# Kernel optimization log

Measured on AMD Instinct MI355X. Metric: run time of the kernel, lower is better.

The kernel has to match this reference:

```python
import jax, jax.numpy as jnp
import numpy as np

IN_FEATURES = 2048
HIDDEN_FEATURES = 8192  # = num_experts * expert_hidden
TOKENS = 16384


def setup_inputs() -> dict:
    key = jax.random.key(0)
    k1, k2, k3, k4 = jax.random.split(key, 4)
    scale = 1.0 / np.sqrt(IN_FEATURES)
    x = jax.random.normal(k1, (TOKENS, IN_FEATURES), dtype=jnp.float32)
    w1 = jax.random.normal(k2, (HIDDEN_FEATURES, IN_FEATURES), dtype=jnp.float32) * scale
    w2 = jax.random.normal(k3, (HIDDEN_FEATURES, IN_FEATURES), dtype=jnp.float32) * scale
    w3 = jax.random.normal(k4, (HIDDEN_FEATURES, IN_FEATURES), dtype=jnp.float32) * scale
    return {"x": x, "w1": w1, "w2": w2, "w3": w3, "num_experts": 8}


def reference(x, w1, w2, w3, num_experts):
    # Block-sparse MoE SwiGLU FFN. Tokens are sorted by expert and balanced:
    # token block e uses hidden slice e of w1/w2/w3 (the stk topology).
    tokens, d = x.shape
    hidden = w1.shape[0]
    e = num_experts
    h_e = hidden // e            # per-expert hidden size
    t_e = tokens // e            # tokens per expert
    xe = x.reshape(e, t_e, d)                  # [E, Te, D]
    w1e = w1.reshape(e, h_e, d)                # [E, He, D]
    w2e = w2.reshape(e, h_e, d)
    w3e = w3.reshape(e, h_e, d)
    # sdd: sparse output of x @ w^T restricted to each token's expert block
    h1 = jnp.einsum("etd,ehd->eth", xe, w1e)   # [E, Te, He]
    h2 = jnp.einsum("etd,ehd->eth", xe, w2e)
    g = jax.nn.silu(h1) * h2                   # fused SiLU gating
    # dsd: block-sparse @ dense w3 -> dense [tokens, D]
    out = jnp.einsum("eth,ehd->etd", g, w3e)
    return out.reshape(tokens, d)
```

## Files before the change

kernel.cpp:

```cpp
#include <hip/hip_runtime.h>
#include <stdint.h>


#define NEXP   8
#define TOKENS 16384
#define D_IN   2048
#define HIDDEN 8192
#define T_E    2048
#define H_E    1024

typedef __attribute__((ext_vector_type(8))) __bf16 bf16x8;
typedef __attribute__((ext_vector_type(4))) float  f32x4;

__device__ __forceinline__ void async_ld16(const void* g, void* l) {
  __builtin_amdgcn_global_load_lds(
      (const __attribute__((address_space(1))) void*)g,
      (__attribute__((address_space(3))) void*)l, 16, 0, 0);
}

__device__ __forceinline__ unsigned short f2bf(float f) {
  union { float f; uint32_t u; } c; c.f = f;
  uint32_t u = c.u;
  u += 0x7FFFu + ((u >> 16) & 1u);
  return (unsigned short)(u >> 16);
}

__device__ __forceinline__ void tile_swizzle(int s, int& mt, int& nt) {
  int g  = s >> 4;
  int w  = s & 15;
  int gm = g & 3, gn = g >> 2;
  int wm = w & 3, wn = w >> 2;
  mt = gm * 4 + wm;
  nt = gn * 4 + wn;
}

__global__ __launch_bounds__(256) void cvt_kernel(
    const float* __restrict__ in, unsigned short* __restrict__ out, int n4) {
  int i = blockIdx.x * 256 + threadIdx.x;
  if (i >= n4) return;
  float4 v = ((const float4*)in)[i];
  ushort4 r;
  r.x = f2bf(v.x); r.y = f2bf(v.y); r.z = f2bf(v.z); r.w = f2bf(v.w);
  ((ushort4*)out)[i] = r;
}

__global__ __launch_bounds__(256) void transpose_w3_kernel(
    const float* __restrict__ w3, unsigned short* __restrict__ w3t) {
  __shared__ unsigned short tile[32][33];
  const int d0 = blockIdx.x * 32;
  const int h0 = blockIdx.y * 32;
  const int tx = threadIdx.x;
  const int ty = threadIdx.y;
#pragma unroll
  for (int j = 0; j < 32; j += 8)
    tile[ty + j][tx] = f2bf(w3[(size_t)(h0 + ty + j) * D_IN + d0 + tx]);
  __syncthreads();
  const int e   = h0 >> 10;
  const int hl0 = h0 & 1023;
#pragma unroll
  for (int j = 0; j < 32; j += 8)
    w3t[((size_t)e * D_IN + d0 + ty + j) * H_E + hl0 + tx] = tile[tx][ty + j];
}

__global__ __launch_bounds__(256) void gemm1_kernel(
    const unsigned short* __restrict__ xb,
    const unsigned short* __restrict__ w1b,
    const unsigned short* __restrict__ w2b,
    unsigned short* __restrict__ g)
{
  __shared__ unsigned short As[128 * 32];
  __shared__ unsigned short B1s[64 * 32];
  __shared__ unsigned short B2s[64 * 32];

  const int bid = blockIdx.x;
  const int e   = bid & 7;
  const int s   = bid >> 3;
  int mt, nt;
  tile_swizzle(s, mt, nt);
  const int m0 = mt * 128;
  const int n0 = nt * 64;

  const unsigned short* A  = xb  + (size_t)e * T_E * D_IN;
  const unsigned short* B1 = w1b + (size_t)e * H_E * D_IN;
  const unsigned short* B2 = w2b + (size_t)e * H_E * D_IN;

  const int tid  = threadIdx.x;
  const int wave = tid >> 6;
  const int lane = tid & 63;
  const int wm   = wave >> 1;
  const int wn   = wave & 1;
  const int srow = lane >> 2;
  const int scol = (lane & 3) * 8;
  const int lm   = lane & 15;
  const int q8   = (lane >> 4) * 8;

  f32x4 acc1[4][2], acc2[4][2];
#pragma unroll
  for (int mi = 0; mi < 4; ++mi)
#pragma unroll
    for (int ni = 0; ni < 2; ++ni) {
      acc1[mi][ni] = (f32x4){0.f, 0.f, 0.f, 0.f};
      acc2[mi][ni] = (f32x4){0.f, 0.f, 0.f, 0.f};
    }

  for (int k0 = 0; k0 < D_IN; k0 += 32) {
    __syncthreads();
#pragma unroll
    for (int j = 0; j < 2; ++j) {
      int r = (wave * 2 + j) * 16 + srow;
      async_ld16(A + (size_t)(m0 + r) * D_IN + k0 + scol,
                 (char*)As + (wave * 2 + j) * 1024 + lane * 16);
    }
    {
      int r = wave * 16 + srow;
      async_ld16(B1 + (size_t)(n0 + r) * D_IN + k0 + scol,
                 (char*)B1s + wave * 1024 + lane * 16);
      async_ld16(B2 + (size_t)(n0 + r) * D_IN + k0 + scol,
                 (char*)B2s + wave * 1024 + lane * 16);
    }
    __syncthreads();

    bf16x8 af[4], b1f[2], b2f[2];
#pragma unroll
    for (int mi = 0; mi < 4; ++mi)
      af[mi] = *(const bf16x8*)(As + (wm * 64 + mi * 16 + lm) * 32 + q8);
#pragma unroll
    for (int ni = 0; ni < 2; ++ni) {
      b1f[ni] = *(const bf16x8*)(B1s + (wn * 32 + ni * 16 + lm) * 32 + q8);
      b2f[ni] = *(const bf16x8*)(B2s + (wn * 32 + ni * 16 + lm) * 32 + q8);
    }
#pragma unroll
    for (int mi = 0; mi < 4; ++mi)
#pragma unroll
      for (int ni = 0; ni < 2; ++ni) {
        acc1[mi][ni] = __builtin_amdgcn_mfma_f32_16x16x32_bf16(
            af[mi], b1f[ni], acc1[mi][ni], 0, 0, 0);
        acc2[mi][ni] = __builtin_amdgcn_mfma_f32_16x16x32_bf16(
            af[mi], b2f[ni], acc2[mi][ni], 0, 0, 0);
      }
  }

  unsigned short* grow = g + (size_t)e * T_E * H_E;
  const int q4 = (lane >> 4) * 4;
#pragma unroll
  for (int mi = 0; mi < 4; ++mi)
#pragma unroll
    for (int ni = 0; ni < 2; ++ni)
#pragma unroll
      for (int r = 0; r < 4; ++r) {
        int row = m0 + wm * 64 + mi * 16 + q4 + r;
        int col = n0 + wn * 32 + ni * 16 + lm;
        float v1 = acc1[mi][ni][r];
        float v2 = acc2[mi][ni][r];
        float gv = (v1 / (1.0f + __expf(-v1))) * v2;
        grow[(size_t)row * H_E + col] = f2bf(gv);
      }
}

__global__ __launch_bounds__(256) void gemm2_kernel(
    const unsigned short* __restrict__ g,
    const unsigned short* __restrict__ w3t,
    float* __restrict__ out)
{
  __shared__ unsigned short As[128 * 32];
  __shared__ unsigned short Bs[128 * 32];

  const int bid = blockIdx.x;
  const int e   = bid & 7;
  const int s   = bid >> 3;
  int mt, nt;
  tile_swizzle(s, mt, nt);
  const int m0 = mt * 128;
  const int n0 = nt * 128;

  const unsigned short* A = g   + (size_t)e * T_E * H_E;
  const unsigned short* B = w3t + (size_t)e * D_IN * H_E;

  const int tid  = threadIdx.x;
  const int wave = tid >> 6;
  const int lane = tid & 63;
  const int wm   = wave >> 1;
  const int wn   = wave & 1;
  const int srow = lane >> 2;
  const int scol = (lane & 3) * 8;
  const int lm   = lane & 15;
  const int q8   = (lane >> 4) * 8;

  f32x4 acc[4][4];
#pragma unroll
  for (int mi = 0; mi < 4; ++mi)
#pragma unroll
    for (int ni = 0; ni < 4; ++ni) acc[mi][ni] = (f32x4){0.f, 0.f, 0.f, 0.f};

  for (int k0 = 0; k0 < H_E; k0 += 32) {
    __syncthreads();
#pragma unroll
    for (int j = 0; j < 2; ++j) {
      int r = (wave * 2 + j) * 16 + srow;
      async_ld16(A + (size_t)(m0 + r) * H_E + k0 + scol,
                 (char*)As + (wave * 2 + j) * 1024 + lane * 16);
      async_ld16(B + (size_t)(n0 + r) * H_E + k0 + scol,
                 (char*)Bs + (wave * 2 + j) * 1024 + lane * 16);
    }
    __syncthreads();

    bf16x8 af[4], bfr[4];
#pragma unroll
    for (int mi = 0; mi < 4; ++mi)
      af[mi] = *(const bf16x8*)(As + (wm * 64 + mi * 16 + lm) * 32 + q8);
#pragma unroll
    for (int ni = 0; ni < 4; ++ni)
      bfr[ni] = *(const bf16x8*)(Bs + (wn * 64 + ni * 16 + lm) * 32 + q8);
#pragma unroll
    for (int mi = 0; mi < 4; ++mi)
#pragma unroll
      for (int ni = 0; ni < 4; ++ni)
        acc[mi][ni] = __builtin_amdgcn_mfma_f32_16x16x32_bf16(
            af[mi], bfr[ni], acc[mi][ni], 0, 0, 0);
  }

  const int q4 = (lane >> 4) * 4;
  float* orow = out + (size_t)e * T_E * D_IN;
#pragma unroll
  for (int mi = 0; mi < 4; ++mi)
#pragma unroll
    for (int ni = 0; ni < 4; ++ni)
#pragma unroll
      for (int r = 0; r < 4; ++r) {
        int row = m0 + wm * 64 + mi * 16 + q4 + r;
        int col = n0 + wn * 64 + ni * 16 + lm;
        orow[(size_t)row * D_IN + col] = acc[mi][ni][r];
      }
}

extern "C" void kernel_launch(void* const* d_in, const int* in_sizes, int n_in,
                              void* d_out, int out_size, void* d_ws, size_t ws_size,
                              hipStream_t stream) {
  const float* x  = (const float*)d_in[0];
  const float* w1 = (const float*)d_in[1];
  const float* w2 = (const float*)d_in[2];
  const float* w3 = (const float*)d_in[3];
  float* out = (float*)d_out;

  char* ws = (char*)d_ws;
  unsigned short* xb  = (unsigned short*)(ws);
  unsigned short* w1b = (unsigned short*)(ws + 67108864);
  unsigned short* w2b = (unsigned short*)(ws + 100663296);
  unsigned short* w3t = (unsigned short*)(ws + 134217728);
  unsigned short* gbuf= (unsigned short*)(ws + 167772160);

  cvt_kernel<<<(TOKENS * D_IN / 4 + 255) / 256, 256, 0, stream>>>(x, xb, TOKENS * D_IN / 4);
  cvt_kernel<<<(HIDDEN * D_IN / 4 + 255) / 256, 256, 0, stream>>>(w1, w1b, HIDDEN * D_IN / 4);
  cvt_kernel<<<(HIDDEN * D_IN / 4 + 255) / 256, 256, 0, stream>>>(w2, w2b, HIDDEN * D_IN / 4);

  transpose_w3_kernel<<<dim3(D_IN / 32, HIDDEN / 32), dim3(32, 8), 0, stream>>>(w3, w3t);

  gemm1_kernel<<<NEXP * 256, 256, 0, stream>>>(xb, w1b, w2b, gbuf);

  gemm2_kernel<<<NEXP * 256, 256, 0, stream>>>(gbuf, w3t, out);
}
```

Baseline: 657.3 us.

## Enlarge GEMM tiles with 4-stage async LDS pipeline and swizzled layout

Both GEMM kernels move to 512-thread blocks with larger output tiles (256x128 and 256x256) to raise arithmetic intensity per loaded byte. The single-buffered loop that synced twice per k-step becomes a 4-slot LDS ring. Loads are issued three stages ahead, and explicit vmcnt waits plus one barrier per step replace the double __syncthreads. An XOR swizzle on LDS chunks cuts bank conflicts, and setprio raises priority around the MFMA block. This adds 128KB of dynamic LDS per block, which limits occupancy to one block per CU, and it raises register pressure from the larger accumulator arrays.

```diff
diff --git a/kernel.cpp b/kernel.cpp
--- a/kernel.cpp
+++ b/kernel.cpp
@@ -25,13 +25,10 @@
   return (unsigned short)(u >> 16);
 }
 
-__device__ __forceinline__ void tile_swizzle(int s, int& mt, int& nt) {
-  int g  = s >> 4;
-  int w  = s & 15;
-  int gm = g & 3, gn = g >> 2;
-  int wm = w & 3, wn = w >> 2;
-  mt = gm * 4 + wm;
-  nt = gn * 4 + wn;
+__device__ __forceinline__ void tile_map(int s, int& mt, int& nt) {
+  int g = s >> 2, w = s & 3;
+  mt = (g & 3) * 2 + (w & 1);
+  nt = (g >> 2) * 2 + (w >> 1);
 }
 
 __global__ __launch_bounds__(256) void cvt_kernel(
@@ -62,75 +59,102 @@
     w3t[((size_t)e * D_IN + d0 + ty + j) * H_E + hl0 + tx] = tile[tx][ty + j];
 }
 
-__global__ __launch_bounds__(256) void gemm1_kernel(
+__global__ __launch_bounds__(512, 2) void gemm1_kernel(
     const unsigned short* __restrict__ xb,
     const unsigned short* __restrict__ w1b,
     const unsigned short* __restrict__ w2b,
     unsigned short* __restrict__ g)
 {
-  __shared__ unsigned short As[128 * 32];
-  __shared__ unsigned short B1s[64 * 32];
-  __shared__ unsigned short B2s[64 * 32];
+  extern __shared__ char lds[];
+  char* const AsB  = lds;
+  char* const B1sB = lds + 65536;
+  char* const B2sB = lds + 98304;
 
   const int bid = blockIdx.x;
   const int e   = bid & 7;
-  const int s   = bid >> 3;
-  int mt, nt;
-  tile_swizzle(s, mt, nt);
-  const int m0 = mt * 128;
-  const int n0 = nt * 64;
-
-  const unsigned short* A  = xb  + (size_t)e * T_E * D_IN;
-  const unsigned short* B1 = w1b + (size_t)e * H_E * D_IN;
-  const unsigned short* B2 = w2b + (size_t)e * H_E * D_IN;
+  int mt, nt; tile_map(bid >> 3, mt, nt);
+  const int m0 = mt * 256;
+  const int n0 = nt * 128;
+
+  const unsigned short* A  = xb  + (size_t)e * T_E * D_IN + (size_t)m0 * D_IN;
+  const unsigned short* B1 = w1b + (size_t)e * H_E * D_IN + (size_t)n0 * D_IN;
+  const unsigned short* B2 = w2b + (size_t)e * H_E * D_IN + (size_t)n0 * D_IN;
 
   const int tid  = threadIdx.x;
   const int wave = tid >> 6;
   const int lane = tid & 63;
-  const int wm   = wave >> 1;
-  const int wn   = wave & 1;
-  const int srow = lane >> 2;
-  const int scol = (lane & 3) * 8;
+  const int wm   = wave >> 2;
+  const int wn   = wave & 3;
   const int lm   = lane & 15;
-  const int q8   = (lane >> 4) * 8;
-
-  f32x4 acc1[4][2], acc2[4][2];
-#pragma unroll
-  for (int mi = 0; mi < 4; ++mi)
+  const int qs   = lane >> 4;
+
+  const int srow   = tid >> 2;
+  const int schunk = tid & 3;
+  const int sc     = (schunk ^ ((srow >> 1) & 3)) * 8;
+  const unsigned short* aS0 = A  + (size_t)srow * D_IN + sc;
+  const unsigned short* aS1 = A  + (size_t)(128 + srow) * D_IN + sc;
+  const unsigned short* b1S = B1 + (size_t)srow * D_IN + sc;
+  const unsigned short* b2S = B2 + (size_t)srow * D_IN + sc;
+  char* const ldsA0 = AsB  + tid * 16;
+  char* const ldsA1 = AsB  + 8192 + tid * 16;
+  char* const ldsB1 = B1sB + tid * 16;
+  char* const ldsB2 = B2sB + tid * 16;
+
+  int offA[8], offB[2];
+#pragma unroll
+  for (int mi = 0; mi < 8; ++mi) {
+    int r = wm * 128 + mi * 16 + lm;
+    offA[mi] = r * 64 + ((qs ^ ((r >> 1) & 3)) * 16);
+  }
+#pragma unroll
+  for (int ni = 0; ni < 2; ++ni) {
+    int r = wn * 32 + ni * 16 + lm;
+    offB[ni] = r * 64 + ((qs ^ ((r >> 1) & 3)) * 16);
+  }
+
+  f32x4 acc1[8][2], acc2[8][2];
+#pragma unroll
+  for (int mi = 0; mi < 8; ++mi)
 #pragma unroll
     for (int ni = 0; ni < 2; ++ni) {
       acc1[mi][ni] = (f32x4){0.f, 0.f, 0.f, 0.f};
       acc2[mi][ni] = (f32x4){0.f, 0.f, 0.f, 0.f};
     }
 
-  for (int k0 = 0; k0 < D_IN; k0 += 32) {
-    __syncthreads();
-#pragma unroll
-    for (int j = 0; j < 2; ++j) {
-      int r = (wave * 2 + j) * 16 + srow;
-      async_ld16(A + (size_t)(m0 + r) * D_IN + k0 + scol,
-                 (char*)As + (wave * 2 + j) * 1024 + lane * 16);
+#define G1_STAGE(t)                                          \
+  { const int sl_ = (t) & 3;                                 \
+    async_ld16(aS0 + (t) * 32, ldsA0 + sl_ * 16384);         \
+    async_ld16(aS1 + (t) * 32, ldsA1 + sl_ * 16384);         \
+    async_ld16(b1S + (t) * 32, ldsB1 + sl_ * 8192);          \
+    async_ld16(b2S + (t) * 32, ldsB2 + sl_ * 8192); }
+
+  G1_STAGE(0); G1_STAGE(1); G1_STAGE(2);
+
+  const int NT = D_IN / 32;
+  for (int t = 0; t < NT; ++t) {
+    if (t < NT - 2)       asm volatile("s_waitcnt vmcnt(8)" ::: "memory");
+    else if (t == NT - 2) asm volatile("s_waitcnt vmcnt(4)" ::: "memory");
+    else                  asm volatile("s_waitcnt vmcnt(0)" ::: "memory");
+    __builtin_amdgcn_s_barrier();
+    __builtin_amdgcn_sched_barrier(0);
+    if (t + 3 < NT) { G1_STAGE(t + 3); }
+
+    const char* At  = AsB  + (t & 3) * 16384;
+    const char* B1t = B1sB + (t & 3) * 8192;
+    const char* B2t = B2sB + (t & 3) * 8192;
+    bf16x8 af[8], b1f[2], b2f[2];
+#pragma unroll
+    for (int ni = 0; ni < 2; ++ni) {
+      b1f[ni] = *(const bf16x8*)(B1t + offB[ni]);
+      b2f[ni] = *(const bf16x8*)(B2t + offB[ni]);
     }
-    {
-      int r = wave * 16 + srow;
-      async_ld16(B1 + (size_t)(n0 + r) * D_IN + k0 + scol,
-                 (char*)B1s + wave * 1024 + lane * 16);
-      async_ld16(B2 + (size_t)(n0 + r) * D_IN + k0 + scol,
-                 (char*)B2s + wave * 1024 + lane * 16);
-    }
-    __syncthreads();
-
-    bf16x8 af[4], b1f[2], b2f[2];
-#pragma unroll
-    for (int mi = 0; mi < 4; ++mi)
-      af[mi] = *(const bf16x8*)(As + (wm * 64 + mi * 16 + lm) * 32 + q8);
-#pragma unroll
-    for (int ni = 0; ni < 2; ++ni) {
-      b1f[ni] = *(const bf16x8*)(B1s + (wn * 32 + ni * 16 + lm) * 32 + q8);
-      b2f[ni] = *(const bf16x8*)(B2s + (wn * 32 + ni * 16 + lm) * 32 + q8);
-    }
-#pragma unroll
-    for (int mi = 0; mi < 4; ++mi)
+#pragma unroll
+    for (int mi = 0; mi < 8; ++mi)
+      af[mi] = *(const bf16x8*)(At + offA[mi]);
+
+    __builtin_amdgcn_s_setprio(1);
+#pragma unroll
+    for (int mi = 0; mi < 8; ++mi)
 #pragma unroll
       for (int ni = 0; ni < 2; ++ni) {
         acc1[mi][ni] = __builtin_amdgcn_mfma_f32_16x16x32_bf16(
@@ -138,99 +162,141 @@
         acc2[mi][ni] = __builtin_amdgcn_mfma_f32_16x16x32_bf16(
             af[mi], b2f[ni], acc2[mi][ni], 0, 0, 0);
       }
-  }
+    __builtin_amdgcn_s_setprio(0);
+    asm volatile("s_waitcnt lgkmcnt(0)" ::: "memory");
+    __builtin_amdgcn_sched_barrier(0);
+  }
+#undef G1_STAGE
 
   unsigned short* grow = g + (size_t)e * T_E * H_E;
-  const int q4 = (lane >> 4) * 4;
-#pragma unroll
-  for (int mi = 0; mi < 4; ++mi)
-#pragma unroll
-    for (int ni = 0; ni < 2; ++ni)
+  const int q4 = qs * 4;
+#pragma unroll
+  for (int mi = 0; mi < 8; ++mi) {
+    const int row = m0 + wm * 128 + mi * 16 + q4;
+#pragma unroll
+    for (int ni = 0; ni < 2; ++ni) {
+      const int col = n0 + wn * 32 + ni * 16 + lm;
 #pragma unroll
       for (int r = 0; r < 4; ++r) {
-        int row = m0 + wm * 64 + mi * 16 + q4 + r;
-        int col = n0 + wn * 32 + ni * 16 + lm;
         float v1 = acc1[mi][ni][r];
         float v2 = acc2[mi][ni][r];
         float gv = (v1 / (1.0f + __expf(-v1))) * v2;
-        grow[(size_t)row * H_E + col] = f2bf(gv);
+        grow[(size_t)(row + r) * H_E + col] = f2bf(gv);
       }
-}
-
-__global__ __launch_bounds__(256) void gemm2_kernel(
+    }
+  }
+}
+
+__global__ __launch_bounds__(512, 2) void gemm2_kernel(
     const unsigned short* __restrict__ g,
     const unsigned short* __restrict__ w3t,
     float* __restrict__ out)
 {
-  __shared__ unsigned short As[128 * 32];
-  __shared__ unsigned short Bs[128 * 32];
+  extern __shared__ char lds[];
+  char* const AsB = lds;
+  char* const BsB = lds + 65536;
 
   const int bid = blockIdx.x;
   const int e   = bid & 7;
-  const int s   = bid >> 3;
-  int mt, nt;
-  tile_swizzle(s, mt, nt);
-  const int m0 = mt * 128;
-  const int n0 = nt * 128;
-
-  const unsigned short* A = g   + (size_t)e * T_E * H_E;
-  const unsigned short* B = w3t + (size_t)e * D_IN * H_E;
+  int mt, nt; tile_map(bid >> 3, mt, nt);
+  const int m0 = mt * 256;
+  const int n0 = nt * 256;
+
+  const unsigned short* A = g   + (size_t)e * T_E * H_E  + (size_t)m0 * H_E;
+  const unsigned short* B = w3t + (size_t)e * D_IN * H_E + (size_t)n0 * H_E;
 
   const int tid  = threadIdx.x;
   const int wave = tid >> 6;
   const int lane = tid & 63;
-  const int wm   = wave >> 1;
-  const int wn   = wave & 1;
-  const int srow = lane >> 2;
-  const int scol = (lane & 3) * 8;
+  const int wm   = wave >> 2;
+  const int wn   = wave & 3;
   const int lm   = lane & 15;
-  const int q8   = (lane >> 4) * 8;
-
-  f32x4 acc[4][4];
-#pragma unroll
-  for (int mi = 0; mi < 4; ++mi)
+  const int qs   = lane >> 4;
+
+  const int srow   = tid >> 2;
+  const int schunk = tid & 3;
+  const int sc     = (schunk ^ ((srow >> 1) & 3)) * 8;
+  const unsigned short* aS0 = A + (size_t)srow * H_E + sc;
+  const unsigned short* aS1 = A + (size_t)(128 + srow) * H_E + sc;
+  const unsigned short* bS0 = B + (size_t)srow * H_E + sc;
+  const unsigned short* bS1 = B + (size_t)(128 + srow) * H_E + sc;
+  char* const ldsA0 = AsB + tid * 16;
+  char* const ldsA1 = AsB + 8192 + tid * 16;
+  char* const ldsB0 = BsB + tid * 16;
+  char* const ldsB1 = BsB + 8192 + tid * 16;
+
+  int offA[8], offB[4];
+#pragma unroll
+  for (int mi = 0; mi < 8; ++mi) {
+    int r = wm * 128 + mi * 16 + lm;
+    offA[mi] = r * 64 + ((qs ^ ((r >> 1) & 3)) * 16);
+  }
+#pragma unroll
+  for (int ni = 0; ni < 4; ++ni) {
+    int r = wn * 64 + ni * 16 + lm;
+    offB[ni] = r * 64 + ((qs ^ ((r >> 1) & 3)) * 16);
+  }
+
+  f32x4 acc[8][4];
+#pragma unroll
+  for (int mi = 0; mi < 8; ++mi)
 #pragma unroll
     for (int ni = 0; ni < 4; ++ni) acc[mi][ni] = (f32x4){0.f, 0.f, 0.f, 0.f};
 
-  for (int k0 = 0; k0 < H_E; k0 += 32) {
-    __syncthreads();
-#pragma unroll
-    for (int j = 0; j < 2; ++j) {
-      int r = (wave * 2 + j) * 16 + srow;
-      async_ld16(A + (size_t)(m0 + r) * H_E + k0 + scol,
-                 (char*)As + (wave * 2 + j) * 1024 + lane * 16);
-      async_ld16(B + (size_t)(n0 + r) * H_E + k0 + scol,
-                 (char*)Bs + (wave * 2 + j) * 1024 + lane * 16);
-    }
-    __syncthreads();
-
-    bf16x8 af[4], bfr[4];
-#pragma unroll
-    for (int mi = 0; mi < 4; ++mi)
-      af[mi] = *(const bf16x8*)(As + (wm * 64 + mi * 16 + lm) * 32 + q8);
+#define G2_STAGE(t)                                          \
+  { const int sl_ = (t) & 3;                                 \
+    async_ld16(aS0 + (t) * 32, ldsA0 + sl_ * 16384);         \
+    async_ld16(aS1 + (t) * 32, ldsA1 + sl_ * 16384);         \
+    async_ld16(bS0 + (t) * 32, ldsB0 + sl_ * 16384);         \
+    async_ld16(bS1 + (t) * 32, ldsB1 + sl_ * 16384); }
+
+  G2_STAGE(0); G2_STAGE(1); G2_STAGE(2);
+
+  const int NT = H_E / 32;
+  for (int t = 0; t < NT; ++t) {
+    if (t < NT - 2)       asm volatile("s_waitcnt vmcnt(8)" ::: "memory");
+    else if (t == NT - 2) asm volatile("s_waitcnt vmcnt(4)" ::: "memory");
+    else                  asm volatile("s_waitcnt vmcnt(0)" ::: "memory");
+    __builtin_amdgcn_s_barrier();
+    __builtin_amdgcn_sched_barrier(0);
+    if (t + 3 < NT) { G2_STAGE(t + 3); }
+
+    const char* At = AsB + (t & 3) * 16384;
+    const char* Bt = BsB + (t & 3) * 16384;
+    bf16x8 af[8], bfr[4];
 #pragma unroll
     for (int ni = 0; ni < 4; ++ni)
-      bfr[ni] = *(const bf16x8*)(Bs + (wn * 64 + ni * 16 + lm) * 32 + q8);
-#pragma unroll
-    for (int mi = 0; mi < 4; ++mi)
+      bfr[ni] = *(const bf16x8*)(Bt + offB[ni]);
+#pragma unroll
+    for (int mi = 0; mi < 8; ++mi)
+      af[mi] = *(const bf16x8*)(At + offA[mi]);
+
+    __builtin_amdgcn_s_setprio(1);
+#pragma unroll
+    for (int mi = 0; mi < 8; ++mi)
 #pragma unroll
       for (int ni = 0; ni < 4; ++ni)
         acc[mi][ni] = __builtin_amdgcn_mfma_f32_16x16x32_bf16(
             af[mi], bfr[ni], acc[mi][ni], 0, 0, 0);
-  }
-
-  const int q4 = (lane >> 4) * 4;
+    __builtin_amdgcn_s_setprio(0);
+    asm volatile("s_waitcnt lgkmcnt(0)" ::: "memory");
+    __builtin_amdgcn_sched_barrier(0);
+  }
+#undef G2_STAGE
+
   float* orow = out + (size_t)e * T_E * D_IN;
-#pragma unroll
-  for (int mi = 0; mi < 4; ++mi)
-#pragma unroll
-    for (int ni = 0; ni < 4; ++ni)
-#pragma unroll
-      for (int r = 0; r < 4; ++r) {
-        int row = m0 + wm * 64 + mi * 16 + q4 + r;
-        int col = n0 + wn * 64 + ni * 16 + lm;
-        orow[(size_t)row * D_IN + col] = acc[mi][ni][r];
-      }
+  const int q4 = qs * 4;
+#pragma unroll
+  for (int mi = 0; mi < 8; ++mi) {
+    const int row = m0 + wm * 128 + mi * 16 + q4;
+#pragma unroll
+    for (int ni = 0; ni < 4; ++ni) {
+      const int col = n0 + wn * 64 + ni * 16 + lm;
+#pragma unroll
+      for (int r = 0; r < 4; ++r)
+        orow[(size_t)(row + r) * D_IN + col] = acc[mi][ni][r];
+    }
+  }
 }
 
 extern "C" void kernel_launch(void* const* d_in, const int* in_sizes, int n_in,
@@ -242,6 +308,15 @@
   const float* w3 = (const float*)d_in[3];
   float* out = (float*)d_out;
 
+  static bool attr_done = false;
+  if (!attr_done) {
+    hipFuncSetAttribute(reinterpret_cast<const void*>(gemm1_kernel),
+                        hipFuncAttributeMaxDynamicSharedMemorySize, 131072);
+    hipFuncSetAttribute(reinterpret_cast<const void*>(gemm2_kernel),
+                        hipFuncAttributeMaxDynamicSharedMemorySize, 131072);
+    attr_done = true;
+  }
+
   char* ws = (char*)d_ws;
   unsigned short* xb  = (unsigned short*)(ws);
   unsigned short* w1b = (unsigned short*)(ws + 67108864);
@@ -255,7 +330,7 @@
 
   transpose_w3_kernel<<<dim3(D_IN / 32, HIDDEN / 32), dim3(32, 8), 0, stream>>>(w3, w3t);
 
-  gemm1_kernel<<<NEXP * 256, 256, 0, stream>>>(xb, w1b, w2b, gbuf);
-
-  gemm2_kernel<<<NEXP * 256, 256, 0, stream>>>(gbuf, w3t, out);
-}
+  gemm1_kernel<<<NEXP * 64, 512, 131072, stream>>>(xb, w1b, w2b, gbuf);
+
+  gemm2_kernel<<<NEXP * 64, 512, 131072, stream>>>(gbuf, w3t, out);
+}
```

Result: faster. 564.0 us (-14.2%).
